# Kernel optimization log

Measured on AMD Instinct MI355X. Metric: run time of the kernel, lower is better.

The kernel has to match this reference:

```python
import jax, jax.numpy as jnp
import numpy as np

B, T, H = 8, 2048, 512


def _minimaxn(x):
    # global min-max normalization (NetTransform.minimaxn)
    mx = jnp.max(x)
    mn = jnp.min(x)
    return (x - mn) / (mx - mn)


def _fb(e):
    # NetTransform.fb, mode='batch', vectorized over the batch.
    # e: (B, 1, T) -> (B, 1, T, T)
    # Result: out[b,0,i,j] = prod(e[b,0,j:i]) for i>j, 1 on diag, 0 above diag.
    x = e[:, 0]                                   # (B, T)
    Bsz, Tsz = x.shape
    X = jnp.broadcast_to(x[:, :, None], (Bsz, Tsz, Tsz))  # xs = x.unsqueeze(-1).repeat(1,1,T)
    tril1 = jnp.tril(jnp.ones((Tsz, Tsz), x.dtype))
    m_f = jnp.triu(jnp.ones((Tsz, Tsz), x.dtype), 1)
    A = X * tril1 + m_f                           # tril(x) + m_f
    C = jnp.cumprod(A, axis=1)                    # cumprod along dim -2
    S = jnp.concatenate([jnp.ones((Bsz, 1, Tsz), x.dtype), C[:, :-1]], axis=1) - m_f
    return S[:, None]                             # (B, 1, T, T)


def _clustering(energy_t):
    # NetTransform.clustering (tnum == 1), vectorized over batch.
    # energy_t: (B, 1, T) -> bool mask (B, 1, T) with top-num_neg of (1-energy) set True
    x = 1.0 - energy_t[:, 0]                      # (B, T)
    num_neg = x.sum(-1).astype(jnp.int32)         # int() truncation; x >= 0 so == floor
    ranks = jnp.argsort(jnp.argsort(-x, axis=-1), axis=-1)  # rank 0 = largest
    m = ranks < num_neg[:, None]
    return m[:, None]                             # (B, 1, T)


def setup_inputs() -> dict:
    key = jax.random.key(0)
    k1, k2, k3 = jax.random.split(key, 3)
    e = jax.random.uniform(k1, (B, 1, T), dtype=jnp.float32)
    h = jax.random.normal(k2, (B, 1, T, H), dtype=jnp.float32)
    ilens = jnp.concatenate([
        jnp.array([T], dtype=jnp.int32),
        jax.random.randint(k3, (B - 1,), T // 2, T + 1).astype(jnp.int32),
    ])
    return {"e": e, "h": h, "ilens": ilens}


def reference(e, h, ilens):
    sg = jax.lax.stop_gradient
    # energy_t = minimaxn(flows['e']).detach()
    energy_t = sg(_minimaxn(e))                   # (B, 1, T)
    # clustering mask (computed in forward; unused when cutting_gauge == 0)
    _ = _clustering(energy_t)
    # energy_t_cumprod = fb(energy_t)  (under no_grad)
    K = sg(_fb(energy_t))                         # (B, 1, T, T)
    # h_agg = (K @ h) / K.sum(-1, keepdim), then transpose(-2, -1)
    h_agg = jnp.einsum('bnts,bnsh->bnth', K, h) / K.sum(-1, keepdims=True)
    h_agg = jnp.swapaxes(h_agg, -2, -1)           # (B, 1, H, T)
    # kernel = (h @ h_agg.detach() + h.detach() @ h_agg) / 2 / sqrt(H)
    kernel = (jnp.matmul(h, sg(h_agg)) + jnp.matmul(sg(h), h_agg)) / 2.0 / np.sqrt(H).astype(np.float32)
    return kernel                                 # (B, 1, T, T)
```

## Files before the change

### kernel.cpp

```cpp
#include <hip/hip_runtime.h>
#include <hip/hip_bf16.h>
#include <stdint.h>

#define B_DIM 8
#define T_DIM 2048
#define H_DIM 512
#define NC 32
#define LCH 64
#define NSUB 4
#define LSUB 16
#define NSEG (NC * NSUB)
#define NOCT 8
#define BM 128
#define BN 128
#define BK 64

typedef float floatx4 __attribute__((ext_vector_type(4)));
typedef __bf16 bf16x4 __attribute__((ext_vector_type(4)));
typedef __bf16 bf16x8 __attribute__((ext_vector_type(8)));

__global__ __launch_bounds__(1024) void minmax_kernel(const float* __restrict__ e,
                                                      float* __restrict__ stats) {
    const float4* e4 = (const float4*)e;
    int tid = threadIdx.x;
    float mn = 1e30f, mx = -1e30f;
    #pragma unroll
    for (int i = 0; i < 4; ++i) {
        float4 v = e4[tid + i * 1024];
        mn = fminf(mn, fminf(fminf(v.x, v.y), fminf(v.z, v.w)));
        mx = fmaxf(mx, fmaxf(fmaxf(v.x, v.y), fmaxf(v.z, v.w)));
    }
    for (int off = 32; off > 0; off >>= 1) {
        mn = fminf(mn, __shfl_down(mn, off, 64));
        mx = fmaxf(mx, __shfl_down(mx, off, 64));
    }
    __shared__ float smn[16], smx[16];
    int wid = tid >> 6;
    if ((tid & 63) == 0) { smn[wid] = mn; smx[wid] = mx; }
    __syncthreads();
    if (tid == 0) {
        mn = smn[0]; mx = smx[0];
        #pragma unroll
        for (int w = 1; w < 16; ++w) { mn = fminf(mn, smn[w]); mx = fmaxf(mx, smx[w]); }
        stats[0] = mn;
        stats[1] = 1.0f / (mx - mn);
    }
}

__global__ __launch_bounds__(512) void chunk_sum_kernel(
        const float* __restrict__ e, const float* __restrict__ h,
        const float* __restrict__ stats,
        __hip_bfloat16* __restrict__ h_bf,
        float* __restrict__ Lsub, float* __restrict__ PPsub, float* __restrict__ LDsub) {
    const int b = blockIdx.x, c = blockIdx.y;
    const int tid = threadIdx.x;
    const int hdq = tid & 127, sub = tid >> 7;
    const int hd = hdq * 4;
    const int t0 = c * LCH + sub * LSUB;

    __shared__ float se[LCH];
    if (tid < LCH) {
        int t = c * LCH + tid;
        se[tid] = (t == 0) ? 0.0f : (e[b * T_DIM + t - 1] - stats[0]) * stats[1];
    }
    __syncthreads();

    const float* hp = h + ((size_t)b * T_DIM + t0) * H_DIM + hd;
    __hip_bfloat16* hbp = h_bf + ((size_t)b * T_DIM + t0) * H_DIM + hd;

    floatx4 lv = {0.0f, 0.0f, 0.0f, 0.0f};
    float ldv = 0.0f, pp = 1.0f;
    #pragma unroll 8
    for (int i = 0; i < LSUB; ++i) {
        float a = se[sub * LSUB + i];
        floatx4 hv = *(const floatx4*)(hp + (size_t)i * H_DIM);
        lv = a * lv + hv;
        ldv = fmaf(a, ldv, 1.0f);
        pp *= a;
        bf16x4 o;
        #pragma unroll
        for (int k = 0; k < 4; ++k) o[k] = (__bf16)hv[k];
        *(bf16x4*)(hbp + (size_t)i * H_DIM) = o;
    }
    int seg = (b * NC + c) * NSUB + sub;
    *(floatx4*)(Lsub + (size_t)seg * H_DIM + hd) = lv;
    if (hdq == 0) { PPsub[seg] = pp; LDsub[seg] = ldv; }
}

__global__ __launch_bounds__(512) void octet_kernel(
        const float* __restrict__ Lsub, const float* __restrict__ PPsub,
        const float* __restrict__ LDsub,
        float* __restrict__ Loct, float* __restrict__ Poct, float* __restrict__ LDoct) {
    const int b = blockIdx.x, o = blockIdx.y, hd = threadIdx.x;
    float lc = 0.0f, ldc = 0.0f, P = 1.0f;
    #pragma unroll 4
    for (int i = 0; i < 16; ++i) {
        int seg = b * NSEG + o * 16 + i;
        float pe = PPsub[seg];
        lc  = fmaf(pe, lc,  Lsub[(size_t)seg * H_DIM + hd]);
        ldc = fmaf(pe, ldc, LDsub[seg]);
        P *= pe;
    }
    int oc = b * NOCT + o;
    Loct[(size_t)oc * H_DIM + hd] = lc;
    if (hd == 0) { Poct[oc] = P; LDoct[oc] = ldc; }
}

__global__ __launch_bounds__(512) void octfold_kernel(
        const float* __restrict__ Loct, const float* __restrict__ Poct,
        const float* __restrict__ LDoct,
        float* __restrict__ Soct, float* __restrict__ SDoct) {
    const int b = blockIdx.x, hd = threadIdx.x;
    float s = 0.0f, sd = 0.0f;
    #pragma unroll
    for (int o = 0; o < NOCT; ++o) {
        int oc = b * NOCT + o;
        Soct[(size_t)oc * H_DIM + hd] = s;
        if (hd == 0) SDoct[oc] = sd;
        float P = Poct[oc];
        s  = fmaf(P, s,  Loct[(size_t)oc * H_DIM + hd]);
        sd = fmaf(P, sd, LDoct[oc]);
    }
}

__global__ __launch_bounds__(512) void segfold_kernel(
        const float* __restrict__ Lsub, const float* __restrict__ PPsub,
        const float* __restrict__ LDsub,
        const float* __restrict__ Soct, const float* __restrict__ SDoct,
        float* __restrict__ Ssub, float* __restrict__ SDsub) {
    const int b = blockIdx.x, o = blockIdx.y, hd = threadIdx.x;
    int oc = b * NOCT + o;
    float s = Soct[(size_t)oc * H_DIM + hd];
    float sd = SDoct[oc];
    #pragma unroll 4
    for (int i = 0; i < 16; ++i) {
        int seg = b * NSEG + o * 16 + i;
        Ssub[(size_t)seg * H_DIM + hd] = s;
        if (hd == 0) SDsub[seg] = sd;
        float pe = PPsub[seg];
        s  = fmaf(pe, s,  Lsub[(size_t)seg * H_DIM + hd]);
        sd = fmaf(pe, sd, LDsub[seg]);
    }
}

__global__ __launch_bounds__(512) void rescan_kernel(
        const float* __restrict__ e, const __hip_bfloat16* __restrict__ h_bf,
        const float* __restrict__ stats,
        const float* __restrict__ Ssub, const float* __restrict__ SDsub,
        __hip_bfloat16* __restrict__ hagg_bf) {
    const int b = blockIdx.x, c = blockIdx.y;
    const int tid = threadIdx.x;
    const int hdq = tid & 127, sub = tid >> 7;
    const int hd = hdq * 4;
    const int t0 = c * LCH + sub * LSUB;

    __shared__ float se[LCH];
    if (tid < LCH) {
        int t = c * LCH + tid;
        se[tid] = (t == 0) ? 0.0f : (e[b * T_DIM + t - 1] - stats[0]) * stats[1];
    }
    __syncthreads();

    const int seg = (b * NC + c) * NSUB + sub;
    const __hip_bfloat16* hbp = h_bf + ((size_t)b * T_DIM + t0) * H_DIM + hd;
    __hip_bfloat16* hop = hagg_bf + ((size_t)b * T_DIM + t0) * H_DIM + hd;

    floatx4 s = *(const floatx4*)(Ssub + (size_t)seg * H_DIM + hd);
    float sd = SDsub[seg];
    #pragma unroll 8
    for (int i = 0; i < LSUB; ++i) {
        float a = se[sub * LSUB + i];
        bf16x4 hb = *(const bf16x4*)(hbp + (size_t)i * H_DIM);
        floatx4 hv;
        #pragma unroll
        for (int k = 0; k < 4; ++k) hv[k] = (float)hb[k];
        s = a * s + hv;
        sd = fmaf(a, sd, 1.0f);
        float inv = 1.0f / sd;
        bf16x4 o;
        #pragma unroll
        for (int k = 0; k < 4; ++k) o[k] = (__bf16)(s[k] * inv);
        *(bf16x4*)(hop + (size_t)i * H_DIM) = o;
    }
}

__device__ __forceinline__ void async16(const void* g, void* l) {
    __builtin_amdgcn_global_load_lds(
        (__attribute__((address_space(1))) void*)g,
        (__attribute__((address_space(3))) void*)l,
        16, 0, 0);
}

__global__ __launch_bounds__(256) void gemm_kernel(
        const __hip_bfloat16* __restrict__ Abf,
        const __hip_bfloat16* __restrict__ Bbf,
        float* __restrict__ C) {
    __shared__ __align__(16) __hip_bfloat16 As[BM * BK];
    __shared__ __align__(16) __hip_bfloat16 Bs[BN * BK];

    const int id = blockIdx.x + (blockIdx.y << 4) + (blockIdx.z << 8);
    const int b  = id & 7;
    const int tt = id >> 3;
    const int tm = (tt & 15) * BM;
    const int sn = (tt >> 4) * BN;

    const int tid = threadIdx.x;
    const int lane = tid & 63;
    const int wave = tid >> 6;
    const int wm = (wave >> 1) * 64;
    const int wn = (wave & 1) * 64;
    const int l16 = lane & 15;
    const int quad = lane >> 4;

    const int srow = tid >> 3;
    const int sgran = (tid & 7) ^ (srow & 7);
    const __hip_bfloat16* Ag = Abf + ((size_t)b * T_DIM + tm + srow) * H_DIM + sgran * 8;
    const __hip_bfloat16* Bg = Bbf + ((size_t)b * T_DIM + sn + srow) * H_DIM + sgran * 8;
    char* AsB = (char*)As;
    char* BsB = (char*)Bs;

    floatx4 zero = {0.0f, 0.0f, 0.0f, 0.0f};
    floatx4 acc[4][4];
    #pragma unroll
    for (int i = 0; i < 4; ++i)
        #pragma unroll
        for (int j = 0; j < 4; ++j) acc[i][j] = zero;

    for (int kk = 0; kk < H_DIM; kk += BK) {
        __syncthreads();
        #pragma unroll
        for (int q = 0; q < 4; ++q) {
            async16(Ag + (size_t)q * 32 * H_DIM + kk, AsB + q * 4096 + tid * 16);
            async16(Bg + (size_t)q * 32 * H_DIM + kk, BsB + q * 4096 + tid * 16);
        }
        asm volatile("s_waitcnt vmcnt(0)" ::: "memory");
        __syncthreads();

        bf16x8 af[2][4], bfv[2][4];
        #pragma unroll
        for (int ku = 0; ku < 2; ++ku)
            #pragma unroll
            for (int i = 0; i < 4; ++i) {
                int ra = wm + i * 16 + l16;
                int rb = wn + i * 16 + l16;
                int ga = (ku * 4 + quad) ^ (l16 & 7);
                af[ku][i]  = *reinterpret_cast<const bf16x8*>(AsB + ra * 128 + ga * 16);
                bfv[ku][i] = *reinterpret_cast<const bf16x8*>(BsB + rb * 128 + ga * 16);
            }
        #pragma unroll
        for (int ku = 0; ku < 2; ++ku)
            #pragma unroll
            for (int i = 0; i < 4; ++i)
                #pragma unroll
                for (int j = 0; j < 4; ++j)
                    acc[i][j] = __builtin_amdgcn_mfma_f32_16x16x32_bf16(bfv[ku][j], af[ku][i], acc[i][j], 0, 0, 0);
    }

    const float scale = 0.04419417382415922f;
    float* Cp = C + (size_t)b * T_DIM * T_DIM;
    #pragma unroll
    for (int i = 0; i < 4; ++i) {
        int row = tm + wm + i * 16 + l16;
        float* crow = Cp + (size_t)row * T_DIM;
        #pragma unroll
        for (int j = 0; j < 4; ++j) {
            int col = sn + wn + j * 16 + quad * 4;
            floatx4 v;
            #pragma unroll
            for (int r = 0; r < 4; ++r) v[r] = acc[i][j][r] * scale;
            *(floatx4*)(crow + col) = v;
        }
    }
}

extern "C" void kernel_launch(void* const* d_in, const int* in_sizes, int n_in,
                              void* d_out, int out_size, void* d_ws, size_t ws_size,
                              hipStream_t stream) {
    const float* e = (const float*)d_in[0];
    const float* h = (const float*)d_in[1];
    float* out = (float*)d_out;

    char* ws = (char*)d_ws;
    float* stats            = (float*)ws;
    __hip_bfloat16* h_bf    = (__hip_bfloat16*)(ws + 4096);
    __hip_bfloat16* hagg_bf = (__hip_bfloat16*)(ws + 4096 + (16u << 20));
    char* p = ws + 4096 + (32u << 20);
    float* Lsub  = (float*)p;   p += (size_t)B_DIM * NSEG * H_DIM * 4;
    float* Ssub  = (float*)p;   p += (size_t)B_DIM * NSEG * H_DIM * 4;
    float* PPsub = (float*)p;   p += B_DIM * NSEG * 4;
    float* LDsub = (float*)p;   p += B_DIM * NSEG * 4;
    float* SDsub = (float*)p;   p += B_DIM * NSEG * 4;
    float* Loct  = (float*)p;   p += (size_t)B_DIM * NOCT * H_DIM * 4;
    float* Soct  = (float*)p;   p += (size_t)B_DIM * NOCT * H_DIM * 4;
    float* Poct  = (float*)p;   p += B_DIM * NOCT * 4;
    float* LDoct = (float*)p;   p += B_DIM * NOCT * 4;
    float* SDoct = (float*)p;

    minmax_kernel<<<1, 1024, 0, stream>>>(e, stats);
    chunk_sum_kernel<<<dim3(B_DIM, NC), 512, 0, stream>>>(e, h, stats, h_bf, Lsub, PPsub, LDsub);
    octet_kernel<<<dim3(B_DIM, NOCT), 512, 0, stream>>>(Lsub, PPsub, LDsub, Loct, Poct, LDoct);
    octfold_kernel<<<B_DIM, 512, 0, stream>>>(Loct, Poct, LDoct, Soct, SDoct);
    segfold_kernel<<<dim3(B_DIM, NOCT), 512, 0, stream>>>(Lsub, PPsub, LDsub, Soct, SDoct, Ssub, SDsub);
    rescan_kernel<<<dim3(B_DIM, NC), 512, 0, stream>>>(e, h_bf, stats, Ssub, SDsub, hagg_bf);
    gemm_kernel<<<dim3(T_DIM / BM, T_DIM / BN, B_DIM), 256, 0, stream>>>(h_bf, hagg_bf, out);
}
```

Measured before the change: 209.4 us.

## Enlarge GEMM tiles to 256x256 with double-buffered async LDS prefetch

The final GEMM now uses 256x256 output tiles computed by 512 threads, with each wave covering a 128x64 region. It double-buffers LDS, issuing the next K-tile's global-to-LDS loads in pieces interleaved with the MFMA phases, and raises wave priority during MFMA. The goal is to hide load latency and increase operand reuse per LDS byte. In exchange it uses 128KB of LDS and more accumulator registers per thread, and the grid shrinks to 512 blocks, which may hurt occupancy and tail balance.

```diff
diff --git a/kernel.cpp b/kernel.cpp
--- a/kernel.cpp
+++ b/kernel.cpp
@@ -11,8 +11,8 @@
 #define LSUB 16
 #define NSEG (NC * NSUB)
 #define NOCT 8
-#define BM 128
-#define BN 128
+#define BM 256
+#define BN 256
 #define BK 64
 
 typedef float floatx4 __attribute__((ext_vector_type(4)));
@@ -191,24 +191,25 @@
         16, 0, 0);
 }
 
-__global__ __launch_bounds__(256) void gemm_kernel(
+__global__ __launch_bounds__(512, 2) void gemm_kernel(
         const __hip_bfloat16* __restrict__ Abf,
         const __hip_bfloat16* __restrict__ Bbf,
         float* __restrict__ C) {
-    __shared__ __align__(16) __hip_bfloat16 As[BM * BK];
-    __shared__ __align__(16) __hip_bfloat16 Bs[BN * BK];
-
-    const int id = blockIdx.x + (blockIdx.y << 4) + (blockIdx.z << 8);
+    __shared__ __align__(16) char lds[131072];
+    char* AsB = lds;
+    char* BsB = lds + 65536;
+
+    const int id = blockIdx.x + (blockIdx.y << 3) + (blockIdx.z << 6);
     const int b  = id & 7;
     const int tt = id >> 3;
-    const int tm = (tt & 15) * BM;
-    const int sn = (tt >> 4) * BN;
+    const int tm = (tt & 7) * BM;
+    const int sn = (tt >> 3) * BN;
 
     const int tid = threadIdx.x;
     const int lane = tid & 63;
     const int wave = tid >> 6;
-    const int wm = (wave >> 1) * 64;
-    const int wn = (wave & 1) * 64;
+    const int wm = (wave >> 2) * 128;
+    const int wn = (wave & 3) * 64;
     const int l16 = lane & 15;
     const int quad = lane >> 4;
 
@@ -216,50 +217,70 @@
     const int sgran = (tid & 7) ^ (srow & 7);
     const __hip_bfloat16* Ag = Abf + ((size_t)b * T_DIM + tm + srow) * H_DIM + sgran * 8;
     const __hip_bfloat16* Bg = Bbf + ((size_t)b * T_DIM + sn + srow) * H_DIM + sgran * 8;
-    char* AsB = (char*)As;
-    char* BsB = (char*)Bs;
 
     floatx4 zero = {0.0f, 0.0f, 0.0f, 0.0f};
-    floatx4 acc[4][4];
-    #pragma unroll
-    for (int i = 0; i < 4; ++i)
+    floatx4 acc[8][4];
+    #pragma unroll
+    for (int i = 0; i < 8; ++i)
         #pragma unroll
         for (int j = 0; j < 4; ++j) acc[i][j] = zero;
 
-    for (int kk = 0; kk < H_DIM; kk += BK) {
-        __syncthreads();
-        #pragma unroll
-        for (int q = 0; q < 4; ++q) {
-            async16(Ag + (size_t)q * 32 * H_DIM + kk, AsB + q * 4096 + tid * 16);
-            async16(Bg + (size_t)q * 32 * H_DIM + kk, BsB + q * 4096 + tid * 16);
-        }
+    #pragma unroll
+    for (int q = 0; q < 4; ++q) {
+        async16(Ag + (size_t)(q * 64) * H_DIM, AsB + q * 8192 + tid * 16);
+        async16(Bg + (size_t)(q * 64) * H_DIM, BsB + q * 8192 + tid * 16);
+    }
+
+    const int NT = H_DIM / BK;
+    for (int t = 0; t < NT; ++t) {
+        const int cur = t & 1;
         asm volatile("s_waitcnt vmcnt(0)" ::: "memory");
-        __syncthreads();
-
-        bf16x8 af[2][4], bfv[2][4];
-        #pragma unroll
-        for (int ku = 0; ku < 2; ++ku)
+        __builtin_amdgcn_s_barrier();
+
+        const char* Ab = AsB + cur * 32768;
+        const char* Bb = BsB + cur * 32768;
+        bf16x8 bv[4];
+        #pragma unroll
+        for (int p = 0; p < 4; ++p) {
+            const int ku = p >> 1, ih = p & 1;
+            if (ih == 0) {
+                #pragma unroll
+                for (int j = 0; j < 4; ++j) {
+                    int rb = wn + j * 16 + l16;
+                    int gb = (ku * 4 + quad) ^ (l16 & 7);
+                    bv[j] = *reinterpret_cast<const bf16x8*>(Bb + rb * 128 + gb * 16);
+                }
+            }
+            bf16x8 av[4];
             #pragma unroll
-            for (int i = 0; i < 4; ++i) {
-                int ra = wm + i * 16 + l16;
-                int rb = wn + i * 16 + l16;
+            for (int i2 = 0; i2 < 4; ++i2) {
+                int ra = wm + (ih * 4 + i2) * 16 + l16;
                 int ga = (ku * 4 + quad) ^ (l16 & 7);
-                af[ku][i]  = *reinterpret_cast<const bf16x8*>(AsB + ra * 128 + ga * 16);
-                bfv[ku][i] = *reinterpret_cast<const bf16x8*>(BsB + rb * 128 + ga * 16);
+                av[i2] = *reinterpret_cast<const bf16x8*>(Ab + ra * 128 + ga * 16);
             }
-        #pragma unroll
-        for (int ku = 0; ku < 2; ++ku)
+            if (t < NT - 1) {
+                const int kk_ = (t + 1) * BK;
+                const int nb = cur ^ 1;
+                async16(Ag + (size_t)(p * 64) * H_DIM + kk_, AsB + nb * 32768 + p * 8192 + tid * 16);
+                async16(Bg + (size_t)(p * 64) * H_DIM + kk_, BsB + nb * 32768 + p * 8192 + tid * 16);
+            }
+            __builtin_amdgcn_s_barrier();
+            __builtin_amdgcn_s_setprio(1);
             #pragma unroll
-            for (int i = 0; i < 4; ++i)
+            for (int i2 = 0; i2 < 4; ++i2)
                 #pragma unroll
                 for (int j = 0; j < 4; ++j)
-                    acc[i][j] = __builtin_amdgcn_mfma_f32_16x16x32_bf16(bfv[ku][j], af[ku][i], acc[i][j], 0, 0, 0);
+                    acc[ih * 4 + i2][j] = __builtin_amdgcn_mfma_f32_16x16x32_bf16(
+                        bv[j], av[i2], acc[ih * 4 + i2][j], 0, 0, 0);
+            __builtin_amdgcn_s_setprio(0);
+            __builtin_amdgcn_s_barrier();
+        }
     }
 
     const float scale = 0.04419417382415922f;
     float* Cp = C + (size_t)b * T_DIM * T_DIM;
     #pragma unroll
-    for (int i = 0; i < 4; ++i) {
+    for (int i = 0; i < 8; ++i) {
         int row = tm + wm + i * 16 + l16;
         float* crow = Cp + (size_t)row * T_DIM;
         #pragma unroll
@@ -302,5 +323,5 @@
     octfold_kernel<<<B_DIM, 512, 0, stream>>>(Loct, Poct, LDoct, Soct, SDoct);
     segfold_kernel<<<dim3(B_DIM, NOCT), 512, 0, stream>>>(Lsub, PPsub, LDsub, Soct, SDoct, Ssub, SDsub);
     rescan_kernel<<<dim3(B_DIM, NC), 512, 0, stream>>>(e, h_bf, stats, Ssub, SDsub, hagg_bf);
-    gemm_kernel<<<dim3(T_DIM / BM, T_DIM / BN, B_DIM), 256, 0, stream>>>(h_bf, hagg_bf, out);
-}
+    gemm_kernel<<<dim3(8, 8, B_DIM), 512, 0, stream>>>(h_bf, hagg_bf, out);
+}
```

Measured after the change: 217.7 us. +3.9%, slower.

## Fold min-max into scan kernels and drop the segment fold pass

Applied to the files above, without the earlier changes.

Removes the standalone min-max kernel by having each chunk_sum and rescan block recompute the global min-max of e redundantly in shared memory. Replaces the octet and segfold passes with one octet-local prefix kernel that writes partial prefixes, which rescan combines with the octet carry. This cuts two kernel launches and their serial dependencies. In exchange every block re-reads all of e (64 KB) and the scan carry adds a small extra combine step.

```diff
diff --git a/kernel.cpp b/kernel.cpp
--- a/kernel.cpp
+++ b/kernel.cpp
@@ -19,37 +19,39 @@
 typedef __bf16 bf16x4 __attribute__((ext_vector_type(4)));
 typedef __bf16 bf16x8 __attribute__((ext_vector_type(8)));
 
-__global__ __launch_bounds__(1024) void minmax_kernel(const float* __restrict__ e,
-                                                      float* __restrict__ stats) {
+__device__ __forceinline__ void block_minmax(const float* __restrict__ e,
+                                             float* __restrict__ sst ,
+                                             float* __restrict__ smn ,
+                                             float* __restrict__ smx ) {
+    const int tid = threadIdx.x;
     const float4* e4 = (const float4*)e;
-    int tid = threadIdx.x;
     float mn = 1e30f, mx = -1e30f;
     #pragma unroll
-    for (int i = 0; i < 4; ++i) {
-        float4 v = e4[tid + i * 1024];
+    for (int i = 0; i < 8; ++i) {
+        float4 v = e4[tid + i * 512];
         mn = fminf(mn, fminf(fminf(v.x, v.y), fminf(v.z, v.w)));
         mx = fmaxf(mx, fmaxf(fmaxf(v.x, v.y), fmaxf(v.z, v.w)));
     }
+    #pragma unroll
     for (int off = 32; off > 0; off >>= 1) {
         mn = fminf(mn, __shfl_down(mn, off, 64));
         mx = fmaxf(mx, __shfl_down(mx, off, 64));
     }
-    __shared__ float smn[16], smx[16];
-    int wid = tid >> 6;
+    const int wid = tid >> 6;
     if ((tid & 63) == 0) { smn[wid] = mn; smx[wid] = mx; }
     __syncthreads();
     if (tid == 0) {
         mn = smn[0]; mx = smx[0];
         #pragma unroll
-        for (int w = 1; w < 16; ++w) { mn = fminf(mn, smn[w]); mx = fmaxf(mx, smx[w]); }
-        stats[0] = mn;
-        stats[1] = 1.0f / (mx - mn);
-    }
+        for (int w = 1; w < 8; ++w) { mn = fminf(mn, smn[w]); mx = fmaxf(mx, smx[w]); }
+        sst[0] = mn;
+        sst[1] = 1.0f / (mx - mn);
+    }
+    __syncthreads();
 }
 
 __global__ __launch_bounds__(512) void chunk_sum_kernel(
         const float* __restrict__ e, const float* __restrict__ h,
-        const float* __restrict__ stats,
         __hip_bfloat16* __restrict__ h_bf,
         float* __restrict__ Lsub, float* __restrict__ PPsub, float* __restrict__ LDsub) {
     const int b = blockIdx.x, c = blockIdx.y;
@@ -58,10 +60,13 @@
     const int hd = hdq * 4;
     const int t0 = c * LCH + sub * LSUB;
 
+    __shared__ float sst[2], smn[8], smx[8];
     __shared__ float se[LCH];
+    block_minmax(e, sst, smn, smx);
+
     if (tid < LCH) {
         int t = c * LCH + tid;
-        se[tid] = (t == 0) ? 0.0f : (e[b * T_DIM + t - 1] - stats[0]) * stats[1];
+        se[tid] = (t == 0) ? 0.0f : (e[b * T_DIM + t - 1] - sst[0]) * sst[1];
     }
     __syncthreads();
 
@@ -87,23 +92,26 @@
     if (hdq == 0) { PPsub[seg] = pp; LDsub[seg] = ldv; }
 }
 
-__global__ __launch_bounds__(512) void octet_kernel(
+__global__ __launch_bounds__(512) void octprefix_kernel(
         const float* __restrict__ Lsub, const float* __restrict__ PPsub,
         const float* __restrict__ LDsub,
+        float* __restrict__ Spart, float* __restrict__ Ppre, float* __restrict__ SDpart,
         float* __restrict__ Loct, float* __restrict__ Poct, float* __restrict__ LDoct) {
     const int b = blockIdx.x, o = blockIdx.y, hd = threadIdx.x;
-    float lc = 0.0f, ldc = 0.0f, P = 1.0f;
+    float sp = 0.0f, sdp = 0.0f, pp = 1.0f;
     #pragma unroll 4
     for (int i = 0; i < 16; ++i) {
         int seg = b * NSEG + o * 16 + i;
+        Spart[(size_t)seg * H_DIM + hd] = sp;
+        if (hd == 0) { Ppre[seg] = pp; SDpart[seg] = sdp; }
         float pe = PPsub[seg];
-        lc  = fmaf(pe, lc,  Lsub[(size_t)seg * H_DIM + hd]);
-        ldc = fmaf(pe, ldc, LDsub[seg]);
-        P *= pe;
+        sp  = fmaf(pe, sp,  Lsub[(size_t)seg * H_DIM + hd]);
+        sdp = fmaf(pe, sdp, LDsub[seg]);
+        pp *= pe;
     }
     int oc = b * NOCT + o;
-    Loct[(size_t)oc * H_DIM + hd] = lc;
-    if (hd == 0) { Poct[oc] = P; LDoct[oc] = ldc; }
+    Loct[(size_t)oc * H_DIM + hd] = sp;
+    if (hd == 0) { Poct[oc] = pp; LDoct[oc] = sdp; }
 }
 
 __global__ __launch_bounds__(512) void octfold_kernel(
@@ -123,30 +131,11 @@
     }
 }
 
-__global__ __launch_bounds__(512) void segfold_kernel(
-        const float* __restrict__ Lsub, const float* __restrict__ PPsub,
-        const float* __restrict__ LDsub,
-        const float* __restrict__ Soct, const float* __restrict__ SDoct,
-        float* __restrict__ Ssub, float* __restrict__ SDsub) {
-    const int b = blockIdx.x, o = blockIdx.y, hd = threadIdx.x;
-    int oc = b * NOCT + o;
-    float s = Soct[(size_t)oc * H_DIM + hd];
-    float sd = SDoct[oc];
-    #pragma unroll 4
-    for (int i = 0; i < 16; ++i) {
-        int seg = b * NSEG + o * 16 + i;
-        Ssub[(size_t)seg * H_DIM + hd] = s;
-        if (hd == 0) SDsub[seg] = sd;
-        float pe = PPsub[seg];
-        s  = fmaf(pe, s,  Lsub[(size_t)seg * H_DIM + hd]);
-        sd = fmaf(pe, sd, LDsub[seg]);
-    }
-}
-
 __global__ __launch_bounds__(512) void rescan_kernel(
         const float* __restrict__ e, const __hip_bfloat16* __restrict__ h_bf,
-        const float* __restrict__ stats,
-        const float* __restrict__ Ssub, const float* __restrict__ SDsub,
+        const float* __restrict__ Spart, const float* __restrict__ Ppre,
+        const float* __restrict__ SDpart,
+        const float* __restrict__ Soct, const float* __restrict__ SDoct,
         __hip_bfloat16* __restrict__ hagg_bf) {
     const int b = blockIdx.x, c = blockIdx.y;
     const int tid = threadIdx.x;
@@ -154,19 +143,27 @@
     const int hd = hdq * 4;
     const int t0 = c * LCH + sub * LSUB;
 
+    __shared__ float sst[2], smn[8], smx[8];
     __shared__ float se[LCH];
+    block_minmax(e, sst, smn, smx);
+
     if (tid < LCH) {
         int t = c * LCH + tid;
-        se[tid] = (t == 0) ? 0.0f : (e[b * T_DIM + t - 1] - stats[0]) * stats[1];
+        se[tid] = (t == 0) ? 0.0f : (e[b * T_DIM + t - 1] - sst[0]) * sst[1];
     }
     __syncthreads();
 
     const int seg = (b * NC + c) * NSUB + sub;
+    const int oc  = b * NOCT + (c >> 2);
     const __hip_bfloat16* hbp = h_bf + ((size_t)b * T_DIM + t0) * H_DIM + hd;
     __hip_bfloat16* hop = hagg_bf + ((size_t)b * T_DIM + t0) * H_DIM + hd;
 
-    floatx4 s = *(const floatx4*)(Ssub + (size_t)seg * H_DIM + hd);
-    float sd = SDsub[seg];
+    const float pq = Ppre[seg];
+    floatx4 soct  = *(const floatx4*)(Soct  + (size_t)oc  * H_DIM + hd);
+    floatx4 spart = *(const floatx4*)(Spart + (size_t)seg * H_DIM + hd);
+    floatx4 s = pq * soct + spart;
+    float sd = fmaf(pq, SDoct[oc], SDpart[seg]);
+
     #pragma unroll 8
     for (int i = 0; i < LSUB; ++i) {
         float a = se[sub * LSUB + i];
@@ -281,26 +278,27 @@
     float* out = (float*)d_out;
 
     char* ws = (char*)d_ws;
-    float* stats            = (float*)ws;
     __hip_bfloat16* h_bf    = (__hip_bfloat16*)(ws + 4096);
     __hip_bfloat16* hagg_bf = (__hip_bfloat16*)(ws + 4096 + (16u << 20));
     char* p = ws + 4096 + (32u << 20);
     float* Lsub  = (float*)p;   p += (size_t)B_DIM * NSEG * H_DIM * 4;
-    float* Ssub  = (float*)p;   p += (size_t)B_DIM * NSEG * H_DIM * 4;
+    float* Spart = (float*)p;   p += (size_t)B_DIM * NSEG * H_DIM * 4;
     float* PPsub = (float*)p;   p += B_DIM * NSEG * 4;
     float* LDsub = (float*)p;   p += B_DIM * NSEG * 4;
-    float* SDsub = (float*)p;   p += B_DIM * NSEG * 4;
+    float* Ppre  = (float*)p;   p += B_DIM * NSEG * 4;
+    float* SDpart= (float*)p;   p += B_DIM * NSEG * 4;
     float* Loct  = (float*)p;   p += (size_t)B_DIM * NOCT * H_DIM * 4;
     float* Soct  = (float*)p;   p += (size_t)B_DIM * NOCT * H_DIM * 4;
     float* Poct  = (float*)p;   p += B_DIM * NOCT * 4;
     float* LDoct = (float*)p;   p += B_DIM * NOCT * 4;
     float* SDoct = (float*)p;
 
-    minmax_kernel<<<1, 1024, 0, stream>>>(e, stats);
-    chunk_sum_kernel<<<dim3(B_DIM, NC), 512, 0, stream>>>(e, h, stats, h_bf, Lsub, PPsub, LDsub);
-    octet_kernel<<<dim3(B_DIM, NOCT), 512, 0, stream>>>(Lsub, PPsub, LDsub, Loct, Poct, LDoct);
+    chunk_sum_kernel<<<dim3(B_DIM, NC), 512, 0, stream>>>(e, h, h_bf, Lsub, PPsub, LDsub);
+    octprefix_kernel<<<dim3(B_DIM, NOCT), 512, 0, stream>>>(Lsub, PPsub, LDsub,
+                                                            Spart, Ppre, SDpart,
+                                                            Loct, Poct, LDoct);
     octfold_kernel<<<B_DIM, 512, 0, stream>>>(Loct, Poct, LDoct, Soct, SDoct);
-    segfold_kernel<<<dim3(B_DIM, NOCT), 512, 0, stream>>>(Lsub, PPsub, LDsub, Soct, SDoct, Ssub, SDsub);
-    rescan_kernel<<<dim3(B_DIM, NC), 512, 0, stream>>>(e, h_bf, stats, Ssub, SDsub, hagg_bf);
+    rescan_kernel<<<dim3(B_DIM, NC), 512, 0, stream>>>(e, h_bf, Spart, Ppre, SDpart,
+                                                       Soct, SDoct, hagg_bf);
     gemm_kernel<<<dim3(T_DIM / BM, T_DIM / BN, B_DIM), 256, 0, stream>>>(h_bf, hagg_bf, out);
 }
```

Result: no change. 208.1 us (-0.6%).
